# Kernel optimization log

Measured on AMD Instinct MI355X. Metric: run time of the kernel, lower is better.

## Reference

```python
import jax, jax.numpy as jnp
import numpy as np

B, N_PER, F = 4, 4096, 64
RATIO, R, K = 0.5, 0.2, 32
M_PER = int(N_PER * RATIO)  # 2048 sampled points per cloud


def fps_single(p, m):
    """Farthest point sampling on one cloud p:[n,3] -> idx:[m] (deterministic start at 0)."""
    d0 = jnp.sum((p - p[0]) ** 2, axis=-1)  # [n]
    def step(mind, _):
        nxt = jnp.argmax(mind)
        d = jnp.sum((p - p[nxt]) ** 2, axis=-1)
        return jnp.minimum(mind, d), nxt
    _, idxs = jax.lax.scan(step, d0, None, length=m - 1)
    return jnp.concatenate([jnp.zeros((1,), jnp.int32), idxs.astype(jnp.int32)])


def setup_inputs() -> dict:
    key = jax.random.key(0)
    ks = jax.random.split(key, 10)
    x = jax.random.normal(ks[0], (B * N_PER, F), jnp.float32)
    pos = jax.random.uniform(ks[1], (B * N_PER, 3), jnp.float32)
    batch = jnp.repeat(jnp.arange(B, dtype=jnp.int32), N_PER)
    def lin(k, fi, fo):
        return jax.random.normal(k, (fi, fo), jnp.float32) / np.sqrt(fi)
    return {
        "x": x, "pos": pos, "batch": batch,
        "W1": lin(ks[2], F + 3, 64), "b1": jnp.zeros((64,), jnp.float32),
        "W2": lin(ks[3], 64, 64),    "b2": jnp.zeros((64,), jnp.float32),
        "W3": lin(ks[4], 64, 128),   "b3": jnp.zeros((128,), jnp.float32),
        "Wg": lin(ks[5], 128, 128),  "bg": jnp.zeros((128,), jnp.float32),
    }


def reference(x, pos, batch, W1, b1, W2, b2, W3, b3, Wg, bg):
    # batch is sorted with equal-sized clouds -> reshape to [B, n, .]
    posb = pos.reshape(B, N_PER, 3)
    xb = x.reshape(B, N_PER, F)

    # --- FPS per cloud ---
    idx = jax.vmap(lambda p: fps_single(p, M_PER))(posb)          # [B, m]
    q = jax.vmap(lambda p, i: p[i])(posb, idx)                    # [B, m, 3] sampled centers

    # --- radius-kNN: k nearest within radius r (self included, dist 0) ---
    d2 = jnp.sum((q[:, :, None, :] - posb[:, None, :, :]) ** 2, axis=-1)  # [B, m, n]
    neg_d, nidx = jax.lax.top_k(-d2, K)                           # [B, m, K]
    valid = (-neg_d) <= R * R                                     # [B, m, K]

    xn = jax.vmap(lambda xx, ii: xx[ii])(xb, nidx)                # [B, m, K, F]
    pn = jax.vmap(lambda pp, ii: pp[ii])(posb, nidx)              # [B, m, K, 3]
    rel = pn - q[:, :, None, :]                                   # relative positions

    # --- PointNetConv: local_nn on concat(x_j, pos_j - pos_i) ---
    h = jnp.concatenate([xn, rel], axis=-1)                       # [B, m, K, F+3]
    h = jax.nn.relu(h @ W1 + b1)
    h = jax.nn.relu(h @ W2 + b2)
    h = jax.nn.relu(h @ W3 + b3)                                  # [B, m, K, 128]

    # --- masked max aggregation over neighbors ---
    neg_inf = jnp.finfo(h.dtype).min
    h = jnp.where(valid[..., None], h, neg_inf)
    agg = jnp.max(h, axis=2)                                      # [B, m, 128]

    # --- global_nn ---
    out = agg @ Wg + bg                                           # [B, m, 128]

    x_out = out.reshape(B * M_PER, -1)
    pos_out = q.reshape(B * M_PER, 3)
    batch_out = jnp.repeat(jnp.arange(B, dtype=jnp.int32), M_PER)
    return x_out, pos_out, batch_out
```

## Files before the change

kernel.cpp:

```cpp
#include <hip/hip_runtime.h>

typedef unsigned long long u64;
typedef unsigned int u32;

#define NB 4
#define NP 4096
#define MP 2048
#define KN 32
#define FD 64
#define CAP 512
#define PPT 16

__device__ __forceinline__ float dist2(float ax, float ay, float az,
                                       float bx, float by, float bz) {
  float dx = ax - bx, dy = ay - by, dz = az - bz;
  return __fadd_rn(__fadd_rn(__fmul_rn(dx, dx), __fmul_rn(dy, dy)),
                   __fmul_rn(dz, dz));
}

__device__ __forceinline__ void fma16(float* acc, float a, const float4* wp) {
#pragma unroll
  for (int u = 0; u < 4; ++u) {
    float4 wv = wp[u];
    acc[u * 4 + 0] = fmaf(a, wv.x, acc[u * 4 + 0]);
    acc[u * 4 + 1] = fmaf(a, wv.y, acc[u * 4 + 1]);
    acc[u * 4 + 2] = fmaf(a, wv.z, acc[u * 4 + 2]);
    acc[u * 4 + 3] = fmaf(a, wv.w, acc[u * 4 + 3]);
  }
}

__device__ __forceinline__ float wave_max_bcast(float x) {
  int v = __float_as_int(x);
#define DPP_STEP(ctrl)                                                     \
  {                                                                        \
    int o = __builtin_amdgcn_update_dpp(0, v, ctrl, 0xF, 0xF, true);       \
    v = __float_as_int(fmaxf(__int_as_float(v), __int_as_float(o)));       \
  }
  DPP_STEP(0x111)
  DPP_STEP(0x112)
  DPP_STEP(0x114)
  DPP_STEP(0x118)
  DPP_STEP(0x142)
  DPP_STEP(0x143)
#undef DPP_STEP
  return __int_as_float(__builtin_amdgcn_readlane(v, 63));
}

__global__ __launch_bounds__(256) void fps_kernel(const float* __restrict__ pos,
                                                  int* __restrict__ fps_idx) {
  const int b = blockIdx.x;
  const float* p = pos + (size_t)b * NP * 3;
  __shared__ __align__(16) float2 sxy[NP];
  __shared__ float sz[NP];
  __shared__ u64 keys[2][4];
  const int t = threadIdx.x;
  const int w = t >> 6;
  const int lane = t & 63;

  for (int i = t; i < NP; i += 256) {
    sxy[i] = make_float2(p[3 * i + 0], p[3 * i + 1]);
    sz[i] = p[3 * i + 2];
  }
  __syncthreads();

  const int base = t * PPT;
  float cx[PPT], cy[PPT], cz[PPT], mind[PPT];
  const float2 q0 = sxy[0];
  const float q0z = sz[0];
  float maxv = -1.0f;
  int maxi = base;
#pragma unroll
  for (int j = 0; j < PPT; ++j) {
    float2 xy = sxy[base + j];
    cx[j] = xy.x; cy[j] = xy.y; cz[j] = sz[base + j];
    mind[j] = dist2(cx[j], cy[j], cz[j], q0.x, q0.y, q0z);
    if (mind[j] > maxv) { maxv = mind[j]; maxi = base + j; }
  }
  if (t == 0) fps_idx[b * MP] = 0;

  for (int it = 1; it < MP; ++it) {
    const float wmax = wave_max_bcast(maxv);
    const u64 bal = __ballot(maxv == wmax);
    const int winner = (int)__ffsll(bal) - 1;
    if (lane == winner)
      keys[it & 1][w] =
          ((u64)__float_as_uint(wmax) << 32) | (u32)(NP - 1 - maxi);
    __syncthreads();
    const u64 k0 = keys[it & 1][0], k1 = keys[it & 1][1];
    const u64 k2 = keys[it & 1][2], k3 = keys[it & 1][3];
    const u64 ka = (k1 > k0) ? k1 : k0;
    const u64 kb = (k3 > k2) ? k3 : k2;
    const u64 km = (kb > ka) ? kb : ka;
    const int gidx = NP - 1 - (int)(km & 0xFFFFFFFFu);
    if (t == 0) fps_idx[b * MP + it] = gidx;
    const float2 cc = sxy[gidx];
    const float ccz = sz[gidx];
    maxv = -1.0f; maxi = base;
#pragma unroll
    for (int j = 0; j < PPT; ++j) {
      const float d = dist2(cx[j], cy[j], cz[j], cc.x, cc.y, ccz);
      mind[j] = fminf(mind[j], d);
      if (mind[j] > maxv) { maxv = mind[j]; maxi = base + j; }
    }
  }
}

__global__ __launch_bounds__(256) void knn_kernel(const float* __restrict__ pos,
                                                  const int* __restrict__ fps_idx,
                                                  int* __restrict__ nbr,
                                                  float* __restrict__ pos_out,
                                                  float* __restrict__ batch_out) {
  __shared__ u64 list[4][CAP];
  const int t = threadIdx.x;
  const int w = t >> 6;
  const int lane = t & 63;
  const int qg = blockIdx.x * 4 + w;
  const int b = qg >> 11;
  const float* p = pos + (size_t)b * NP * 3;
  const int pidx = fps_idx[qg];
  const float qx = p[3 * pidx], qy = p[3 * pidx + 1], qz = p[3 * pidx + 2];

  int base = 0;
  for (int rnd = 0; rnd < NP / 64; ++rnd) {
    const int j = rnd * 64 + lane;
    const float d2 = dist2(p[3 * j], p[3 * j + 1], p[3 * j + 2], qx, qy, qz);
    const bool pred = (d2 <= 0.04f);
    const u64 bal = __ballot(pred);
    if (pred) {
      const int slot = base + (int)__popcll(bal & ((1ull << lane) - 1ull));
      if (slot < CAP) list[w][slot] = ((u64)__float_as_uint(d2) << 32) | (u32)j;
    }
    base += (int)__popcll(bal);
  }
  const int L = base < CAP ? base : CAP;
  __syncthreads();

  u64 mk[8];
#pragma unroll
  for (int s = 0; s < 8; ++s) {
    const int sl = lane + s * 64;
    mk[s] = (sl < L) ? list[w][sl] : ~0ull;
  }
  u64 lmin = mk[0];
#pragma unroll
  for (int s = 1; s < 8; ++s) lmin = (mk[s] < lmin) ? mk[s] : lmin;

  int myNbr = -1;
  for (int r = 0; r < KN; ++r) {
    u64 m = lmin;
#pragma unroll
    for (int off = 32; off >= 1; off >>= 1) {
      u64 om = __shfl_xor(m, off, 64);
      m = (om < m) ? om : m;
    }
    if (m == ~0ull) break;
    if (lane == r) myNbr = (int)(m & 0xFFFFFFFFu);
    if (lmin == m) {
#pragma unroll
      for (int s = 0; s < 8; ++s) if (mk[s] == m) mk[s] = ~0ull;
      lmin = mk[0];
#pragma unroll
      for (int s = 1; s < 8; ++s) lmin = (mk[s] < lmin) ? mk[s] : lmin;
    }
  }
  if (lane < KN) nbr[(size_t)qg * KN + lane] = myNbr;
  if (lane == 0) {
    pos_out[qg * 3 + 0] = qx;
    pos_out[qg * 3 + 1] = qy;
    pos_out[qg * 3 + 2] = qz;
    batch_out[qg] = (float)b;
  }
}

__global__ __launch_bounds__(256) void mlp_kernel(
    const float* __restrict__ x, const float* __restrict__ pos,
    const int* __restrict__ fps_idx, const int* __restrict__ nbr,
    const float* __restrict__ W1, const float* __restrict__ b1,
    const float* __restrict__ W2, const float* __restrict__ b2,
    const float* __restrict__ W3, const float* __restrict__ b3,
    float* __restrict__ aggG) {
  __shared__ __align__(16) float inB[64][68];
  __shared__ __align__(16) float hB[64][68];
  __shared__ __align__(16) float wB[4352];
  __shared__ u32 agg[2][128];
  __shared__ int vrow[64];
  const int t = threadIdx.x;
  const int q0 = blockIdx.x * 2;

  ((u32*)agg)[t] = 0u;
  for (int i = t; i < 1072; i += 256) ((float4*)wB)[i] = ((const float4*)W1)[i];
  {
    const int r = t >> 2, qu = t & 3;
    const int qg = q0 + (r >> 5);
    const int nid = nbr[(size_t)qg * KN + (r & 31)];
    const int gid = (nid < 0) ? 0 : nid;
    const int bb = qg >> 11;
    const float4* xr =
        (const float4*)(x + ((size_t)bb * NP + gid) * FD + qu * 16);
#pragma unroll
    for (int u = 0; u < 4; ++u) {
      float4 v = xr[u];
      inB[r][qu * 16 + u * 4 + 0] = v.x;
      inB[r][qu * 16 + u * 4 + 1] = v.y;
      inB[r][qu * 16 + u * 4 + 2] = v.z;
      inB[r][qu * 16 + u * 4 + 3] = v.w;
    }
    if (qu == 0) {
      vrow[r] = nid;
      const float* p = pos + (size_t)bb * NP * 3;
      const int pidx = fps_idx[qg];
      inB[r][64] = p[3 * gid + 0] - p[3 * pidx + 0];
      inB[r][65] = p[3 * gid + 1] - p[3 * pidx + 1];
      inB[r][66] = p[3 * gid + 2] - p[3 * pidx + 2];
    }
  }
  __syncthreads();

  const int c0a = (t & 3) * 16;
  const int ra = t >> 2;
  {
    float acc[16];
#pragma unroll
    for (int c = 0; c < 16; ++c) acc[c] = b1[c0a + c];
    for (int k = 0; k < 67; ++k)
      fma16(acc, inB[ra][k], (const float4*)&wB[k * 64 + c0a]);
#pragma unroll
    for (int c = 0; c < 16; ++c) hB[ra][c0a + c] = fmaxf(acc[c], 0.0f);
  }
  __syncthreads();
  for (int i = t; i < 1024; i += 256) ((float4*)wB)[i] = ((const float4*)W2)[i];
  __syncthreads();
  {
    float acc[16];
#pragma unroll
    for (int c = 0; c < 16; ++c) acc[c] = b2[c0a + c];
    for (int k = 0; k < 64; ++k)
      fma16(acc, hB[ra][k], (const float4*)&wB[k * 64 + c0a]);
#pragma unroll
    for (int c = 0; c < 16; ++c) inB[ra][c0a + c] = fmaxf(acc[c], 0.0f);
  }
  __syncthreads();

  const int c0b = (t & 7) * 16;
  const int r0 = (t >> 3) * 2;
  float acc0[16], acc1[16];
#pragma unroll
  for (int c = 0; c < 16; ++c) { acc0[c] = b3[c0b + c]; acc1[c] = b3[c0b + c]; }
  for (int half = 0; half < 2; ++half) {
    for (int i = t; i < 1024; i += 256)
      ((float4*)wB)[i] = ((const float4*)(W3 + half * 32 * 128))[i];
    __syncthreads();
    for (int k = 0; k < 32; ++k) {
      const float a0 = inB[r0][half * 32 + k];
      const float a1 = inB[r0 + 1][half * 32 + k];
      const float4* wp = (const float4*)&wB[k * 128 + c0b];
      fma16(acc0, a0, wp);
      fma16(acc1, a1, wp);
    }
    __syncthreads();
  }
  {
    const int qq = r0 >> 5;
    const int v0 = vrow[r0], v1 = vrow[r0 + 1];
#pragma unroll
    for (int c = 0; c < 16; ++c) {
      float m = 0.0f;
      if (v0 >= 0) m = fmaxf(m, acc0[c]);
      if (v1 >= 0) m = fmaxf(m, acc1[c]);
      atomicMax(&agg[qq][c0b + c], __float_as_uint(m));
    }
  }
  __syncthreads();
  aggG[(size_t)(q0 + (t >> 7)) * 128 + (t & 127)] =
      __uint_as_float(agg[t >> 7][t & 127]);
}

__global__ __launch_bounds__(256) void wg_kernel(const float* __restrict__ aggG,
                                                 const float* __restrict__ Wg,
                                                 const float* __restrict__ bg,
                                                 float* __restrict__ xout) {
  __shared__ __align__(16) float wL[64 * 128];
  __shared__ __align__(16) float aL[32][132];
  const int t = threadIdx.x;
  const size_t row0 = (size_t)blockIdx.x * 32;
  for (int i = t; i < 1024; i += 256) {
    const int r = i >> 5, qd = i & 31;
    float4 v = ((const float4*)(aggG + (row0 + r) * 128))[qd];
    *((float4*)&aL[r][qd * 4]) = v;
  }
  const int r = t >> 3;
  const int c0 = (t & 7) * 16;
  float acc[16];
#pragma unroll
  for (int c = 0; c < 16; ++c) acc[c] = bg[c0 + c];
  for (int half = 0; half < 2; ++half) {
    __syncthreads();
    for (int i = t; i < 2048; i += 256)
      ((float4*)wL)[i] = ((const float4*)(Wg + half * 64 * 128))[i];
    __syncthreads();
    for (int k = 0; k < 64; ++k)
      fma16(acc, aL[r][half * 64 + k], (const float4*)&wL[k * 128 + c0]);
  }
#pragma unroll
  for (int u = 0; u < 4; ++u) {
    float4 v = make_float4(acc[u * 4 + 0], acc[u * 4 + 1], acc[u * 4 + 2],
                           acc[u * 4 + 3]);
    ((float4*)(xout + (row0 + r) * 128 + c0))[u] = v;
  }
}


extern "C" void kernel_launch(void* const* d_in, const int* in_sizes, int n_in,
                              void* d_out, int out_size, void* d_ws,
                              size_t ws_size, hipStream_t stream) {
  const float* x   = (const float*)d_in[0];
  const float* pos = (const float*)d_in[1];
  const float* W1 = (const float*)d_in[3];
  const float* b1 = (const float*)d_in[4];
  const float* W2 = (const float*)d_in[5];
  const float* b2 = (const float*)d_in[6];
  const float* W3 = (const float*)d_in[7];
  const float* b3 = (const float*)d_in[8];
  const float* Wg = (const float*)d_in[9];
  const float* bg = (const float*)d_in[10];

  float* out = (float*)d_out;
  float* x_out = out;
  float* pos_out = out + (size_t)NB * MP * 128;
  float* batch_out = pos_out + (size_t)NB * MP * 3;

  char* ws = (char*)d_ws;
  int* fps_idx = (int*)ws;
  int* nbr = (int*)(ws + 32768);
  float* aggG = (float*)(ws + 32768 + (size_t)NB * MP * KN * 4);

  hipLaunchKernelGGL(fps_kernel, dim3(NB), dim3(256), 0, stream, pos, fps_idx);
  hipLaunchKernelGGL(knn_kernel, dim3(NB * MP / 4), dim3(256), 0, stream, pos,
                     fps_idx, nbr, pos_out, batch_out);
  hipLaunchKernelGGL(mlp_kernel, dim3(NB * MP / 2), dim3(256), 0, stream, x,
                     pos, fps_idx, nbr, W1, b1, W2, b2, W3, b3, aggG);
  hipLaunchKernelGGL(wg_kernel, dim3(NB * MP / 32), dim3(256), 0, stream, aggG,
                     Wg, bg, x_out);
}
```

Before: 1.384 ms.

## Carry winner coordinates through FPS reduction instead of LDS position lookup

The FPS kernel no longer stages every point in shared memory. Each thread loads its 16 points straight into registers with vectorized float4 loads. During the argmax reduction, the winning thread publishes its point's coordinates together with its distance, so the next centre comes from the small record array rather than a dependent LDS gather indexed by the winner. This removes one dependent LDS load from each of the 2047 serial iterations, at the cost of a register mux tree per iteration to select the local max point. Ties between waves now resolve by wave order (lower wave wins) rather than through the packed key encoding.

```diff
diff --git a/kernel.cpp b/kernel.cpp
--- a/kernel.cpp
+++ b/kernel.cpp
@@ -50,57 +50,96 @@
                                                   int* __restrict__ fps_idx) {
   const int b = blockIdx.x;
   const float* p = pos + (size_t)b * NP * 3;
-  __shared__ __align__(16) float2 sxy[NP];
-  __shared__ float sz[NP];
-  __shared__ u64 keys[2][4];
+  __shared__ __align__(16) float4 recV[2][4];
+  __shared__ __align__(16) int recI[2][4];
   const int t = threadIdx.x;
   const int w = t >> 6;
   const int lane = t & 63;
-
-  for (int i = t; i < NP; i += 256) {
-    sxy[i] = make_float2(p[3 * i + 0], p[3 * i + 1]);
-    sz[i] = p[3 * i + 2];
-  }
-  __syncthreads();
-
   const int base = t * PPT;
+
   float cx[PPT], cy[PPT], cz[PPT], mind[PPT];
-  const float2 q0 = sxy[0];
-  const float q0z = sz[0];
+  {
+    const float4* P4 = (const float4*)(p + (size_t)base * 3);
+    float f[48];
+#pragma unroll
+    for (int u = 0; u < 12; ++u) {
+      float4 v = P4[u];
+      f[4 * u + 0] = v.x; f[4 * u + 1] = v.y;
+      f[4 * u + 2] = v.z; f[4 * u + 3] = v.w;
+    }
+#pragma unroll
+    for (int j = 0; j < PPT; ++j) {
+      cx[j] = f[3 * j + 0]; cy[j] = f[3 * j + 1]; cz[j] = f[3 * j + 2];
+    }
+  }
+
+  const float q0x = p[0], q0y = p[1], q0z = p[2];
   float maxv = -1.0f;
-  int maxi = base;
+  int maxj = 0;
 #pragma unroll
   for (int j = 0; j < PPT; ++j) {
-    float2 xy = sxy[base + j];
-    cx[j] = xy.x; cy[j] = xy.y; cz[j] = sz[base + j];
-    mind[j] = dist2(cx[j], cy[j], cz[j], q0.x, q0.y, q0z);
-    if (mind[j] > maxv) { maxv = mind[j]; maxi = base + j; }
+    const float d = dist2(cx[j], cy[j], cz[j], q0x, q0y, q0z);
+    mind[j] = d;
+    if (d > maxv) { maxv = d; maxj = j; }
   }
   if (t == 0) fps_idx[b * MP] = 0;
 
   for (int it = 1; it < MP; ++it) {
+    const bool b0 = (maxj & 1) != 0, b1 = (maxj & 2) != 0;
+    const bool b2 = (maxj & 4) != 0, b3 = (maxj & 8) != 0;
+    float ax[8], ay[8], az[8];
+#pragma unroll
+    for (int u = 0; u < 8; ++u) {
+      ax[u] = b0 ? cx[2 * u + 1] : cx[2 * u];
+      ay[u] = b0 ? cy[2 * u + 1] : cy[2 * u];
+      az[u] = b0 ? cz[2 * u + 1] : cz[2 * u];
+    }
+#pragma unroll
+    for (int u = 0; u < 4; ++u) {
+      ax[u] = b1 ? ax[2 * u + 1] : ax[2 * u];
+      ay[u] = b1 ? ay[2 * u + 1] : ay[2 * u];
+      az[u] = b1 ? az[2 * u + 1] : az[2 * u];
+    }
+#pragma unroll
+    for (int u = 0; u < 2; ++u) {
+      ax[u] = b2 ? ax[2 * u + 1] : ax[2 * u];
+      ay[u] = b2 ? ay[2 * u + 1] : ay[2 * u];
+      az[u] = b2 ? az[2 * u + 1] : az[2 * u];
+    }
+    ax[0] = b3 ? ax[1] : ax[0];
+    ay[0] = b3 ? ay[1] : ay[0];
+    az[0] = b3 ? az[1] : az[0];
+
     const float wmax = wave_max_bcast(maxv);
     const u64 bal = __ballot(maxv == wmax);
-    const int winner = (int)__ffsll(bal) - 1;
-    if (lane == winner)
-      keys[it & 1][w] =
-          ((u64)__float_as_uint(wmax) << 32) | (u32)(NP - 1 - maxi);
-    __syncthreads();
-    const u64 k0 = keys[it & 1][0], k1 = keys[it & 1][1];
-    const u64 k2 = keys[it & 1][2], k3 = keys[it & 1][3];
-    const u64 ka = (k1 > k0) ? k1 : k0;
-    const u64 kb = (k3 > k2) ? k3 : k2;
-    const u64 km = (kb > ka) ? kb : ka;
-    const int gidx = NP - 1 - (int)(km & 0xFFFFFFFFu);
-    if (t == 0) fps_idx[b * MP + it] = gidx;
-    const float2 cc = sxy[gidx];
-    const float ccz = sz[gidx];
-    maxv = -1.0f; maxi = base;
+    const u64 below = (1ull << lane) - 1ull;
+    if ((maxv == wmax) && ((bal & below) == 0)) {
+      recV[it & 1][w] = make_float4(wmax, ax[0], ay[0], az[0]);
+      recI[it & 1][w] = base + maxj;
+    }
+    __syncthreads();
+
+    const float4 r0 = recV[it & 1][0], r1 = recV[it & 1][1];
+    const float4 r2 = recV[it & 1][2], r3 = recV[it & 1][3];
+    const int4 ri = *(const int4*)recI[it & 1];
+    const bool s01 = r1.x > r0.x, s23 = r3.x > r2.x;
+    const float4 ma = s01 ? r1 : r0;
+    const int ia = s01 ? ri.y : ri.x;
+    const float4 mb = s23 ? r3 : r2;
+    const int ib = s23 ? ri.w : ri.z;
+    const bool sab = mb.x > ma.x;
+    const float4 mm = sab ? mb : ma;
+    const int im = sab ? ib : ia;
+    if (t == 0) fps_idx[b * MP + it] = im;
+
+    const float ccx = mm.y, ccy = mm.z, ccz = mm.w;
+    maxv = -1.0f; maxj = 0;
 #pragma unroll
     for (int j = 0; j < PPT; ++j) {
-      const float d = dist2(cx[j], cy[j], cz[j], cc.x, cc.y, ccz);
-      mind[j] = fminf(mind[j], d);
-      if (mind[j] > maxv) { maxv = mind[j]; maxi = base + j; }
+      const float d = dist2(cx[j], cy[j], cz[j], ccx, ccy, ccz);
+      const float nm = fminf(mind[j], d);
+      mind[j] = nm;
+      if (nm > maxv) { maxv = nm; maxj = j; }
     }
   }
 }
```

New measurement: 4.246 ms. +206.7%, slower.
